# Optimization experiments

Hardware: AMD Instinct MI355X
Metric: run time of the kernel (lower is better)

The kernel has to match this reference:

```python
import jax, jax.numpy as jnp
import numpy as np

BLOCK_SIZE = 3
SOBEL_PAD = 1  # sobel_size // 2
BLOCK_PAD = BLOCK_SIZE // 2

_SOBEL_X = jnp.array([[-1.0, 0.0, 1.0], [-2.0, 0.0, 2.0], [-1.0, 0.0, 1.0]], dtype=jnp.float32)[None, None]
_SOBEL_Y = jnp.array([[-1.0, -2.0, -1.0], [0.0, 0.0, 0.0], [1.0, 2.0, 1.0]], dtype=jnp.float32)[None, None]
_SUM_K = jnp.ones((1, 1, BLOCK_SIZE, BLOCK_SIZE), dtype=jnp.float32)


def _pad_replicate(x, p):
    return jnp.pad(x, ((0, 0), (0, 0), (p, p), (p, p)), mode='edge')


def _conv(x, k):
    return jax.lax.conv_general_dilated(
        x, k, window_strides=(1, 1), padding='VALID',
        dimension_numbers=('NCHW', 'OIHW', 'NCHW'))


def setup_inputs() -> dict:
    key = jax.random.key(0)
    image = jax.random.uniform(key, (8, 1, 1080, 1920), dtype=jnp.float32) * 255.0
    return {"image": image}


def reference(image) -> jnp.ndarray:
    img = image.astype(jnp.float32)
    img_p = _pad_replicate(img, SOBEL_PAD)
    Ix = _conv(img_p, _SOBEL_X)
    Iy = _conv(img_p, _SOBEL_Y)
    Ixx = Ix * Ix
    Iyy = Iy * Iy
    Ixy = Ix * Iy
    sum_Ixx = _conv(_pad_replicate(Ixx, BLOCK_PAD), _SUM_K)
    sum_Iyy = _conv(_pad_replicate(Iyy, BLOCK_PAD), _SUM_K)
    sum_Ixy = _conv(_pad_replicate(Ixy, BLOCK_PAD), _SUM_K)
    half_trace = (sum_Ixx + sum_Iyy) * 0.5
    diff_half = (sum_Ixx - sum_Iyy) * 0.5
    sqrt_disc = jnp.sqrt(diff_half * diff_half + sum_Ixy * sum_Ixy + 1e-10)
    lambda_min = half_trace - sqrt_disc
    return jnp.clip(lambda_min, 0.0)
```

## Files before the change

### kernel.cpp

```cpp
#include <hip/hip_runtime.h>

typedef float v2f __attribute__((ext_vector_type(2)));
typedef float v4f __attribute__((ext_vector_type(4)));

#define IMG_H 1080
#define IMG_W 1920
#define NBATCH 8
#define LSTRIP 9
#define BROWS (4*LSTRIP)
#define NK (LSTRIP+4)


static __device__ __forceinline__ v2f vfma2(v2f a, v2f b, v2f c) {
    return __builtin_elementwise_fma(a, b, c);
}

template<bool EDGE>
__device__ __forceinline__ void st_body(const float* __restrict__ g,
                                        float* __restrict__ outb,
                                        int vb, int s0) {
    const bool eL = EDGE && (vb == 0);
    const bool eR = EDGE && (vb == IMG_W - 4);
    int wb = vb - 4;
    if (EDGE) { if (eL) wb = 0; if (eR) wb = IMG_W - 12; }
    const bool topFix = (s0 == 0);
    const bool botFix = (s0 + LSTRIP == IMG_H);

    v2f R[4][6];
    v2f hdR[3][3], hsR[3][3];
    float hfd[3], hfs[3];
    v2f hxx[3][2], hyy[3][2], hxy[3][2];

    auto issue = [&](int k) {
        int lr = s0 - 2 + k;
        lr = max(0, min(IMG_H - 1, lr));
        const float4* rp = (const float4*)(g + (size_t)lr * IMG_W + wb);
        const float4 A = rp[0], B = rp[1], C = rp[2];
        v2f* r = R[k % 4];
        r[0] = v2f{A.x, A.y}; r[1] = v2f{A.z, A.w};
        r[2] = v2f{B.x, B.y}; r[3] = v2f{B.z, B.w};
        r[4] = v2f{C.x, C.y}; r[5] = v2f{C.z, C.w};
    };

    issue(0); issue(1); issue(2);

    const v2f two = {2.0f, 2.0f};

    #pragma unroll
    for (int k = 0; k < NK; ++k) {
        if (k + 3 < NK) issue(k + 3);

        {
            const v2f* r = R[k % 4];
            v2f Za, Zb, Zc, Zd, Sab, Sbc, Scd;
            if (EDGE) {
                const float rs[12] = {r[0].x, r[0].y, r[1].x, r[1].y,
                                      r[2].x, r[2].y, r[3].x, r[3].y,
                                      r[4].x, r[4].y, r[5].x, r[5].y};
                const float zL[8] = {rs[0],rs[0],rs[0],rs[1],rs[2],rs[3],rs[4],rs[5]};
                const float zR[8] = {rs[6],rs[7],rs[8],rs[9],rs[10],rs[11],rs[11],rs[11]};
                float z[8];
                #pragma unroll
                for (int j = 0; j < 8; ++j)
                    z[j] = eL ? zL[j] : (eR ? zR[j] : rs[j + 2]);
                hfd[k % 3] = eR ? (z[5] - z[4]) : (z[3] - z[2]);
                hfs[k % 3] = eR ? (z[4] + 3.0f * z[5]) : (3.0f * z[2] + z[3]);
                Za = v2f{z[0], z[1]}; Zb = v2f{z[2], z[3]};
                Zc = v2f{z[4], z[5]}; Zd = v2f{z[6], z[7]};
                Sab = v2f{z[1], z[2]}; Sbc = v2f{z[3], z[4]}; Scd = v2f{z[5], z[6]};
            } else {
                Za = r[1]; Zb = r[2]; Zc = r[3]; Zd = r[4];
                Sab = v2f{r[1].y, r[2].x};
                Sbc = v2f{r[2].y, r[3].x};
                Scd = v2f{r[3].y, r[4].x};
            }
            v2f* hd = hdR[k % 3];
            v2f* hs = hsR[k % 3];
            hd[0] = Zb - Za; hd[1] = Zc - Zb; hd[2] = Zd - Zc;
            hs[0] = vfma2(Sab, two, Za) + Zb;
            hs[1] = vfma2(Sbc, two, Zb) + Zc;
            hs[2] = vfma2(Scd, two, Zc) + Zd;
        }

        if (k >= 2) {
            const int rr = k - 2;
            const int sm = rr % 3, sz = (rr + 1) % 3, sp = (rr + 2) % 3;

            v2f Ixp[3], Iyp[3];
            #pragma unroll
            for (int j = 0; j < 3; ++j) {
                Ixp[j] = vfma2(hdR[sz][j], two, hdR[sm][j]) + hdR[sp][j];
                Iyp[j] = hsR[sp][j] - hsR[sm][j];
            }
            if (EDGE) {
                const float ixf = hfd[sm] + 2.0f * hfd[sz] + hfd[sp];
                const float iyf = hfs[sp] - hfs[sm];
                if (eL) { Ixp[0].x = ixf; Iyp[0].x = iyf; }
                if (eR) { Ixp[2].y = ixf; Iyp[2].y = iyf; }
            }

            v2f xx[3], yy[3], xy[3];
            #pragma unroll
            for (int j = 0; j < 3; ++j) {
                xx[j] = Ixp[j] * Ixp[j];
                yy[j] = Iyp[j] * Iyp[j];
                xy[j] = Ixp[j] * Iyp[j];
            }
            {
                v2f* hx = hxx[rr % 3];
                v2f* hy = hyy[rr % 3];
                v2f* hz = hxy[rr % 3];
                hx[0] = xx[0] + v2f{xx[0].y, xx[1].x} + xx[1];
                hx[1] = xx[1] + v2f{xx[1].y, xx[2].x} + xx[2];
                hy[0] = yy[0] + v2f{yy[0].y, yy[1].x} + yy[1];
                hy[1] = yy[1] + v2f{yy[1].y, yy[2].x} + yy[2];
                hz[0] = xy[0] + v2f{xy[0].y, xy[1].x} + xy[1];
                hz[1] = xy[1] + v2f{xy[1].y, xy[2].x} + xy[2];
            }
            if (rr == 1 && topFix) {
                #pragma unroll
                for (int q = 0; q < 2; ++q) {
                    hxx[0][q] = hxx[1][q]; hyy[0][q] = hyy[1][q]; hxy[0][q] = hxy[1][q];
                }
            }
            if (rr == LSTRIP + 1 && botFix) {
                #pragma unroll
                for (int q = 0; q < 2; ++q) {
                    hxx[rr % 3][q] = hxx[(rr - 1) % 3][q];
                    hyy[rr % 3][q] = hyy[(rr - 1) % 3][q];
                    hxy[rr % 3][q] = hxy[(rr - 1) % 3][q];
                }
            }

            if (rr >= 2) {
                const int a = (rr - 2) % 3, b2 = (rr - 1) % 3, c = rr % 3;
                float rv[4];
                #pragma unroll
                for (int q = 0; q < 2; ++q) {
                    const v2f sxx = hxx[a][q] + hxx[b2][q] + hxx[c][q];
                    const v2f syy = hyy[a][q] + hyy[b2][q] + hyy[c][q];
                    const v2f sxy = hxy[a][q] + hxy[b2][q] + hxy[c][q];
                    const v2f S = sxx + syy;
                    const v2f D = sxx - syy;
                    const v2f E = sxy + sxy;
                    const v2f disc = vfma2(D, D, vfma2(E, E, v2f{4e-10f, 4e-10f}));
                    const v2f qv = {__builtin_sqrtf(disc.x), __builtin_sqrtf(disc.y)};
                    const v2f lam = (S - qv) * 0.5f;
                    rv[2 * q]     = fmaxf(lam.x, 0.0f);
                    rv[2 * q + 1] = fmaxf(lam.y, 0.0f);
                }
                float* orowp = outb + (size_t)(s0 + rr - 2) * IMG_W + vb;
                __builtin_nontemporal_store(v4f{rv[0], rv[1], rv[2], rv[3]},
                                            (v4f*)orowp);
            }
        }
    }
}

__global__ __launch_bounds__(256, 3)
void shi_tomasi_kernel(const float* __restrict__ img, float* __restrict__ out) {
    const int cg    = threadIdx.x & 63;
    const int strip = threadIdx.x >> 6;
    const int vb = blockIdx.x * 256 + cg * 4;
    if (vb >= IMG_W) return;
    const int s0 = blockIdx.y * BROWS + strip * LSTRIP;
    const float* g = img + (size_t)blockIdx.z * (IMG_H * IMG_W);
    float* outb = out + (size_t)blockIdx.z * (IMG_H * IMG_W);

    if (blockIdx.x == 0 || blockIdx.x == gridDim.x - 1)
        st_body<true>(g, outb, vb, s0);
    else
        st_body<false>(g, outb, vb, s0);
}

extern "C" void kernel_launch(void* const* d_in, const int* in_sizes, int n_in,
                              void* d_out, int out_size, void* d_ws, size_t ws_size,
                              hipStream_t stream) {
    const float* img = (const float*)d_in[0];
    float* out = (float*)d_out;
    dim3 grid(8, IMG_H / BROWS, NBATCH);
    shi_tomasi_kernel<<<grid, 256, 0, stream>>>(img, out);
}
```

Measured before the change: 121.9 us.

## Share row halos via ds_bpermute instead of redundant overlapping vector loads

Each lane now loads a single float4 per image row and gets its left and right neighbour columns from adjacent lanes with ds_bpermute, instead of issuing three overlapping float4 loads. Blocks are laid out with 240-column overlap so the 4 halo lanes compute but do not store, and one lane fetches the block's left halo from memory. The EDGE template split is removed in favour of runtime edge branches. Stores drop the nontemporal hint, and launch bounds rise to 4 blocks per SM. The goal is fewer global load instructions and registers in exchange for cross-lane permute work, some wasted lanes and extra edge-handling ALU work in every block.

```diff
diff --git a/kernel.cpp b/kernel.cpp
--- a/kernel.cpp
+++ b/kernel.cpp
@@ -14,19 +14,32 @@
 static __device__ __forceinline__ v2f vfma2(v2f a, v2f b, v2f c) {
     return __builtin_elementwise_fma(a, b, c);
 }
+static __device__ __forceinline__ float bperm(int addr, float v) {
+    return __int_as_float(__builtin_amdgcn_ds_bpermute(addr, __float_as_int(v)));
+}
 
-template<bool EDGE>
-__device__ __forceinline__ void st_body(const float* __restrict__ g,
-                                        float* __restrict__ outb,
-                                        int vb, int s0) {
-    const bool eL = EDGE && (vb == 0);
-    const bool eR = EDGE && (vb == IMG_W - 4);
-    int wb = vb - 4;
-    if (EDGE) { if (eL) wb = 0; if (eR) wb = IMG_W - 12; }
+__global__ __launch_bounds__(256, 4)
+void shi_tomasi_kernel(const float* __restrict__ img, float* __restrict__ out) {
+    const int cg    = threadIdx.x & 63;
+    const int strip = threadIdx.x >> 6;
+    const int bx    = blockIdx.x;
+    const int c0    = bx * 240 + cg * 4;
+    const int c0l   = min(c0, IMG_W - 4);
+    const int s0    = blockIdx.y * BROWS + strip * LSTRIP;
+    const float* g  = img + (size_t)blockIdx.z * (IMG_H * IMG_W);
+    float* outb     = out + (size_t)blockIdx.z * (IMG_H * IMG_W);
+
+    const bool eL     = (c0 == 0);
+    const bool eR     = (c0 == IMG_W - 4);
+    const bool hload  = (cg == 0) && (bx > 0);
+    const bool doSt   = (cg < 60);
+    const int  aLft   = 4 * (cg - 1);
+    const int  aRgt   = 4 * (cg + 1);
     const bool topFix = (s0 == 0);
     const bool botFix = (s0 + LSTRIP == IMG_H);
 
-    v2f R[4][6];
+    v4f Zr[4];
+    v2f Hr[4] = {};
     v2f hdR[3][3], hsR[3][3];
     float hfd[3], hfs[3];
     v2f hxx[3][2], hyy[3][2], hxy[3][2];
@@ -34,12 +47,9 @@
     auto issue = [&](int k) {
         int lr = s0 - 2 + k;
         lr = max(0, min(IMG_H - 1, lr));
-        const float4* rp = (const float4*)(g + (size_t)lr * IMG_W + wb);
-        const float4 A = rp[0], B = rp[1], C = rp[2];
-        v2f* r = R[k % 4];
-        r[0] = v2f{A.x, A.y}; r[1] = v2f{A.z, A.w};
-        r[2] = v2f{B.x, B.y}; r[3] = v2f{B.z, B.w};
-        r[4] = v2f{C.x, C.y}; r[5] = v2f{C.z, C.w};
+        const float* rowp = g + (size_t)lr * IMG_W;
+        Zr[k % 4] = *(const v4f*)(rowp + c0l);
+        if (hload) Hr[k % 4] = *(const v2f*)(rowp + (c0 - 2));
     };
 
     issue(0); issue(1); issue(2);
@@ -51,35 +61,27 @@
         if (k + 3 < NK) issue(k + 3);
 
         {
-            const v2f* r = R[k % 4];
-            v2f Za, Zb, Zc, Zd, Sab, Sbc, Scd;
-            if (EDGE) {
-                const float rs[12] = {r[0].x, r[0].y, r[1].x, r[1].y,
-                                      r[2].x, r[2].y, r[3].x, r[3].y,
-                                      r[4].x, r[4].y, r[5].x, r[5].y};
-                const float zL[8] = {rs[0],rs[0],rs[0],rs[1],rs[2],rs[3],rs[4],rs[5]};
-                const float zR[8] = {rs[6],rs[7],rs[8],rs[9],rs[10],rs[11],rs[11],rs[11]};
-                float z[8];
-                #pragma unroll
-                for (int j = 0; j < 8; ++j)
-                    z[j] = eL ? zL[j] : (eR ? zR[j] : rs[j + 2]);
-                hfd[k % 3] = eR ? (z[5] - z[4]) : (z[3] - z[2]);
-                hfs[k % 3] = eR ? (z[4] + 3.0f * z[5]) : (3.0f * z[2] + z[3]);
-                Za = v2f{z[0], z[1]}; Zb = v2f{z[2], z[3]};
-                Zc = v2f{z[4], z[5]}; Zd = v2f{z[6], z[7]};
-                Sab = v2f{z[1], z[2]}; Sbc = v2f{z[3], z[4]}; Scd = v2f{z[5], z[6]};
-            } else {
-                Za = r[1]; Zb = r[2]; Zc = r[3]; Zd = r[4];
-                Sab = v2f{r[1].y, r[2].x};
-                Sbc = v2f{r[2].y, r[3].x};
-                Scd = v2f{r[3].y, r[4].x};
-            }
+            const v4f Z = Zr[k % 4];
+            const float zl0 = bperm(aLft, Z.z), zl1 = bperm(aLft, Z.w);
+            const float zr0 = bperm(aRgt, Z.x), zr1 = bperm(aRgt, Z.y);
+            v2f Z0 = v2f{zl0, zl1};
+            if (cg == 0) Z0 = eL ? v2f{Z.x, Z.x} : Hr[k % 4];
+            const v2f Z1 = v2f{Z.x, Z.y};
+            const v2f Z2 = v2f{Z.z, Z.w};
+            v2f Z3 = v2f{zr0, zr1};
+            if (eR) Z3 = v2f{Z.w, Z.w};
+
+            const v2f Sab = v2f{Z0.y, Z1.x};
+            const v2f Sbc = v2f{Z1.y, Z2.x};
+            const v2f Scd = v2f{Z2.y, Z3.x};
             v2f* hd = hdR[k % 3];
             v2f* hs = hsR[k % 3];
-            hd[0] = Zb - Za; hd[1] = Zc - Zb; hd[2] = Zd - Zc;
-            hs[0] = vfma2(Sab, two, Za) + Zb;
-            hs[1] = vfma2(Sbc, two, Zb) + Zc;
-            hs[2] = vfma2(Scd, two, Zc) + Zd;
+            hd[0] = Z1 - Z0; hd[1] = Z2 - Z1; hd[2] = Z3 - Z2;
+            hs[0] = vfma2(Sab, two, Z0) + Z1;
+            hs[1] = vfma2(Sbc, two, Z1) + Z2;
+            hs[2] = vfma2(Scd, two, Z2) + Z3;
+            hfd[k % 3] = eR ? (Z2.y - Z2.x) : (Z1.y - Z1.x);
+            hfs[k % 3] = eR ? (Z2.x + 3.0f * Z2.y) : (3.0f * Z1.x + Z1.y);
         }
 
         if (k >= 2) {
@@ -92,12 +94,10 @@
                 Ixp[j] = vfma2(hdR[sz][j], two, hdR[sm][j]) + hdR[sp][j];
                 Iyp[j] = hsR[sp][j] - hsR[sm][j];
             }
-            if (EDGE) {
-                const float ixf = hfd[sm] + 2.0f * hfd[sz] + hfd[sp];
-                const float iyf = hfs[sp] - hfs[sm];
-                if (eL) { Ixp[0].x = ixf; Iyp[0].x = iyf; }
-                if (eR) { Ixp[2].y = ixf; Iyp[2].y = iyf; }
-            }
+            const float ixf = hfd[sm] + 2.0f * hfd[sz] + hfd[sp];
+            const float iyf = hfs[sp] - hfs[sm];
+            if (eL) { Ixp[0].x = ixf; Iyp[0].x = iyf; }
+            if (eR) { Ixp[2].y = ixf; Iyp[2].y = iyf; }
 
             v2f xx[3], yy[3], xy[3];
             #pragma unroll
@@ -149,28 +149,13 @@
                     rv[2 * q]     = fmaxf(lam.x, 0.0f);
                     rv[2 * q + 1] = fmaxf(lam.y, 0.0f);
                 }
-                float* orowp = outb + (size_t)(s0 + rr - 2) * IMG_W + vb;
-                __builtin_nontemporal_store(v4f{rv[0], rv[1], rv[2], rv[3]},
-                                            (v4f*)orowp);
+                if (doSt) {
+                    float* orowp = outb + (size_t)(s0 + rr - 2) * IMG_W + c0;
+                    *(v4f*)orowp = v4f{rv[0], rv[1], rv[2], rv[3]};
+                }
             }
         }
     }
-}
-
-__global__ __launch_bounds__(256, 3)
-void shi_tomasi_kernel(const float* __restrict__ img, float* __restrict__ out) {
-    const int cg    = threadIdx.x & 63;
-    const int strip = threadIdx.x >> 6;
-    const int vb = blockIdx.x * 256 + cg * 4;
-    if (vb >= IMG_W) return;
-    const int s0 = blockIdx.y * BROWS + strip * LSTRIP;
-    const float* g = img + (size_t)blockIdx.z * (IMG_H * IMG_W);
-    float* outb = out + (size_t)blockIdx.z * (IMG_H * IMG_W);
-
-    if (blockIdx.x == 0 || blockIdx.x == gridDim.x - 1)
-        st_body<true>(g, outb, vb, s0);
-    else
-        st_body<false>(g, outb, vb, s0);
 }
 
 extern "C" void kernel_launch(void* const* d_in, const int* in_sizes, int n_in,
```

Measured after the change: 120.1 us. Within noise of the previous version (-1.5%).
